# Performance work log

Measured on AMD Instinct MI355X. Metric: run time of the kernel, lower is better.

## Reference

```python
import jax, jax.numpy as jnp
import numpy as np


def _pairwise_dist(x, y):
    # x: [B, N, D], y: [B, M, D] -> [B, N, M] Euclidean distances.
    # Use ||x||^2 + ||y||^2 - 2<x,y> (gram form) to avoid the [B,N,M,D]
    # broadcast intermediate the torch code materializes.
    x2 = jnp.sum(x * x, axis=-1)  # [B, N]
    y2 = jnp.sum(y * y, axis=-1)  # [B, M]
    xy = jnp.einsum('bnd,bmd->bnm', x, y)  # [B, N, M]
    sq = x2[:, :, None] + y2[:, None, :] - 2.0 * xy
    return jnp.sqrt(jnp.maximum(sq, 1e-12))


def setup_inputs() -> dict:
    key = jax.random.key(0)
    k1, k2 = jax.random.split(key)
    B, N, M, D = 8, 4096, 4096, 64
    pred = jax.random.normal(k1, (B, N, D), dtype=jnp.float32)
    label = jax.random.normal(k2, (B, M, D), dtype=jnp.float32)
    return {"pred": pred, "label": label}


def reference(pred, label):
    dis = _pairwise_dist(pred, label)  # [B, N, M]
    dis_xy = jnp.max(jnp.min(dis, axis=2))  # max over all (b, n) of min over m
    dis_yx = jnp.max(jnp.min(dis, axis=1))  # max over all (b, m) of min over n
    return dis_xy + dis_yx
```

## Files before the change

kernel.cpp:

```cpp
#include <hip/hip_runtime.h>
#include <hip/hip_bf16.h>

#define B_ 8
#define N_ 4096
#define M_ 4096
#define D_ 64
#define BNT (B_ * N_)
#define BMT (B_ * M_)
#define TA 128
#define TB 128
#define CHUNK_TILES 8
#define CHUNK_B (TB * CHUNK_TILES)
#define MCHUNK (M_ / CHUNK_B)

typedef short bf16x8 __attribute__((ext_vector_type(8)));
typedef float f32x4 __attribute__((ext_vector_type(4)));

__device__ __forceinline__ unsigned short f2bf(float f) {
  __hip_bfloat16 h = __float2bfloat16(f);
  return *reinterpret_cast<unsigned short*>(&h);
}

__device__ __forceinline__ unsigned fkey(float f) {
  unsigned b = __float_as_uint(f);
  return b ^ ((unsigned)((int)b >> 31) | 0x80000000u);
}
__device__ __forceinline__ float funkey(unsigned k) {
  unsigned b = (k & 0x80000000u) ? (k ^ 0x80000000u) : ~k;
  return __uint_as_float(b);
}

__device__ __forceinline__ bf16x8 cvt8(float4 lo, float4 hi) {
  union { unsigned short u[8]; bf16x8 v; } r;
  r.u[0] = f2bf(lo.x); r.u[1] = f2bf(lo.y); r.u[2] = f2bf(lo.z); r.u[3] = f2bf(lo.w);
  r.u[4] = f2bf(hi.x); r.u[5] = f2bf(hi.y); r.u[6] = f2bf(hi.z); r.u[7] = f2bf(hi.w);
  return r.v;
}

__device__ __forceinline__ void gload_lds16(const void* g, void* l) {
  __builtin_amdgcn_global_load_lds(
      (const __attribute__((address_space(1))) unsigned int*)g,
      (__attribute__((address_space(3))) unsigned int*)l, 16, 0, 0);
}

template <int ROWS, bool BF>
__device__ __forceinline__ void stage_tile(const void* gsrc, unsigned short* lds,
                                           int t, int srcpat) {
  if (BF) {
    constexpr int PER_WAVE = (ROWS * 128 / 1024) / 4;
    const char* gp = (const char*)gsrc;
    int w = t >> 6;
#pragma unroll
    for (int i = 0; i < PER_WAVE; i++) {
      int q = w * PER_WAVE + i;
      gload_lds16(gp + q * 1024 + srcpat, (char*)lds + q * 1024);
    }
  } else {
    const float4* g4 = (const float4*)gsrc;
#pragma unroll
    for (int i = 0; i < ROWS * 16 / 256; i++) {
      int off = i * 256 + t;
      float4 v = g4[off];
      int row = off >> 4;
      int cb = (off & 15) * 8;
      int ba = (row * 128 + cb) ^ ((row & 7) << 4);
      ushort4 p;
      p.x = f2bf(v.x); p.y = f2bf(v.y); p.z = f2bf(v.z); p.w = f2bf(v.w);
      *(ushort4*)((char*)lds + ba) = p;
    }
  }
}

template <bool CONV>
__global__ __launch_bounds__(256) void prep_kernel(
    const float* __restrict__ pred, const float* __restrict__ label,
    unsigned short* __restrict__ predbf, unsigned short* __restrict__ labelbf,
    float* __restrict__ x2, float* __restrict__ y2,
    unsigned* __restrict__ minN, unsigned* __restrict__ minM,
    unsigned* __restrict__ gmax) {
  int t = threadIdx.x;
  int lane = t & 15;
  long row = (long)blockIdx.x * 16 + (t >> 4);
  bool isA = row < BNT;
  const float4* src;
  unsigned short* bdst;
  float* ndst;
  unsigned* mdst;
  if (isA) {
    src = (const float4*)(pred + row * D_);
    bdst = predbf + row * D_;
    ndst = x2 + row;
    mdst = minN + row;
  } else {
    long r2 = row - BNT;
    src = (const float4*)(label + r2 * D_);
    bdst = labelbf + r2 * D_;
    ndst = y2 + r2;
    mdst = minM + r2;
  }
  float4 v = src[lane];
  if (CONV) {
    float s = isA ? -2.f : 1.f;
    ushort4 p;
    p.x = f2bf(s * v.x); p.y = f2bf(s * v.y);
    p.z = f2bf(s * v.z); p.w = f2bf(s * v.w);
    *(ushort4*)(bdst + lane * 4) = p;
  }
  float s = v.x * v.x + v.y * v.y + v.z * v.z + v.w * v.w;
  s += __shfl_xor(s, 1);
  s += __shfl_xor(s, 2);
  s += __shfl_xor(s, 4);
  s += __shfl_xor(s, 8);
  if (lane == 0) {
    *ndst = s;
    *mdst = 0xFFFFFFFFu;
  }
  if (blockIdx.x == 0 && t < 2) gmax[t] = 0u;
}

template <bool BF>
__global__ __launch_bounds__(256) void fused_kernel(
    const void* __restrict__ Asrc, const void* __restrict__ Bsrc,
    const float* __restrict__ x2g, const float* __restrict__ y2g,
    unsigned* __restrict__ minN, unsigned* __restrict__ minM) {
  __shared__ alignas(16) unsigned short Bs[2][TB * 64];
  __shared__ float y2l[CHUNK_B];
  __shared__ float cmSlab[2][CHUNK_B];
  __shared__ float red[2][TA];

  const int t = threadIdx.x;
  const int b = blockIdx.z;
  const int a0 = blockIdx.x * TA;
  const int m0 = blockIdx.y * CHUNK_B;
  const int w = t >> 6, l = t & 63;
  const int g = l >> 4, c = l & 15;
  const int wr = w >> 1, wc = w & 1;
  const int srcpat = (l >> 3) * 128 + (((l & 7) * 16) ^ ((l >> 3) << 4));

  const size_t rowbytes = BF ? 128 : 256;
  const char* Bgl = (const char*)Bsrc + ((size_t)b * M_ + m0) * rowbytes;

  ((float4*)y2l)[t] = ((const float4*)(y2g + (size_t)b * M_ + m0))[t];

  stage_tile<TB, BF>(Bgl, Bs[0], t, srcpat);

  bf16x8 af[2][4];
  if (BF) {
    const unsigned short* Ab =
        (const unsigned short*)Asrc + ((size_t)b * N_ + a0) * D_;
#pragma unroll
    for (int kk = 0; kk < 2; kk++)
#pragma unroll
      for (int mi = 0; mi < 4; mi++)
        af[kk][mi] =
            *(const bf16x8*)(Ab + (size_t)(wr * 64 + mi * 16 + c) * D_ + kk * 32 + g * 8);
  } else {
    const float* Af = (const float*)Asrc + ((size_t)b * N_ + a0) * D_;
#pragma unroll
    for (int kk = 0; kk < 2; kk++)
#pragma unroll
      for (int mi = 0; mi < 4; mi++) {
        const float4* p =
            (const float4*)(Af + (size_t)(wr * 64 + mi * 16 + c) * D_ + kk * 32 + g * 8);
        float4 lo = p[0], hi = p[1];
        lo.x *= -2.f; lo.y *= -2.f; lo.z *= -2.f; lo.w *= -2.f;
        hi.x *= -2.f; hi.y *= -2.f; hi.z *= -2.f; hi.w *= -2.f;
        af[kk][mi] = cvt8(lo, hi);
      }
  }

  float x2v[4][4];
#pragma unroll
  for (int mi = 0; mi < 4; mi++)
#pragma unroll
    for (int e = 0; e < 4; e++)
      x2v[mi][e] = x2g[(size_t)b * N_ + a0 + wr * 64 + mi * 16 + g * 4 + e];

  float rmin[4][4];
#pragma unroll
  for (int mi = 0; mi < 4; mi++)
#pragma unroll
    for (int e = 0; e < 4; e++) rmin[mi][e] = INFINITY;

  __syncthreads();

#pragma unroll
  for (int it = 0; it < CHUNK_TILES; it++) {
    if (it + 1 < CHUNK_TILES)
      stage_tile<TB, BF>(Bgl + (size_t)(it + 1) * TB * rowbytes,
                         Bs[(it + 1) & 1], t, srcpat);
    const char* Bcur = (const char*)Bs[it & 1];

    float nbv[4];
#pragma unroll
    for (int ni = 0; ni < 4; ni++)
      nbv[ni] = y2l[it * TB + wc * 64 + ni * 16 + c];

#pragma unroll
    for (int h = 0; h < 2; h++) {
      bf16x8 b0[2], b1[2];
#pragma unroll
      for (int nj = 0; nj < 2; nj++) {
        int r = wc * 64 + (h * 2 + nj) * 16 + c;
        b0[nj] = *(const bf16x8*)(Bcur + ((r * 128 + g * 16) ^ ((r & 7) << 4)));
        b1[nj] = *(const bf16x8*)(Bcur + ((r * 128 + 64 + g * 16) ^ ((r & 7) << 4)));
      }
      f32x4 acc[4][2];
#pragma unroll
      for (int mi = 0; mi < 4; mi++)
#pragma unroll
        for (int nj = 0; nj < 2; nj++) {
          float nv = nbv[h * 2 + nj];
          acc[mi][nj] = (f32x4){nv, nv, nv, nv};
        }
#pragma unroll
      for (int mi = 0; mi < 4; mi++)
#pragma unroll
        for (int nj = 0; nj < 2; nj++)
          acc[mi][nj] = __builtin_amdgcn_mfma_f32_16x16x32_bf16(
              af[0][mi], b0[nj], acc[mi][nj], 0, 0, 0);
#pragma unroll
      for (int mi = 0; mi < 4; mi++)
#pragma unroll
        for (int nj = 0; nj < 2; nj++)
          acc[mi][nj] = __builtin_amdgcn_mfma_f32_16x16x32_bf16(
              af[1][mi], b1[nj], acc[mi][nj], 0, 0, 0);

#pragma unroll
      for (int nj = 0; nj < 2; nj++) {
        float cm = INFINITY;
#pragma unroll
        for (int mi = 0; mi < 4; mi++)
#pragma unroll
          for (int e = 0; e < 4; e++) {
            float v = acc[mi][nj][e];
            rmin[mi][e] = fminf(rmin[mi][e], v);
            cm = fminf(cm, v + x2v[mi][e]);
          }
        cm = fminf(cm, __shfl_xor(cm, 16));
        cm = fminf(cm, __shfl_xor(cm, 32));
        if (g == 0)
          cmSlab[wr][it * TB + wc * 64 + (h * 2 + nj) * 16 + c] =
              cm - nbv[h * 2 + nj];
      }
    }
    __syncthreads();
  }

#pragma unroll
  for (int mi = 0; mi < 4; mi++)
#pragma unroll
    for (int e = 0; e < 4; e++) {
      float r = rmin[mi][e];
      r = fminf(r, __shfl_xor(r, 1));
      r = fminf(r, __shfl_xor(r, 2));
      r = fminf(r, __shfl_xor(r, 4));
      r = fminf(r, __shfl_xor(r, 8));
      rmin[mi][e] = r;
    }
  if (c == 0) {
#pragma unroll
    for (int mi = 0; mi < 4; mi++)
#pragma unroll
      for (int e = 0; e < 4; e++)
        red[wc][wr * 64 + mi * 16 + g * 4 + e] = rmin[mi][e];
  }
  __syncthreads();
  if (t < TA) {
    float m = fminf(red[0][t], red[1][t]);
    atomicMin(&minN[(size_t)b * N_ + a0 + t], fkey(m));
  }
#pragma unroll
  for (int i = 0; i < CHUNK_B / 256; i++) {
    int r = i * 256 + t;
    float v = fminf(cmSlab[0][r], cmSlab[1][r]);
    atomicMin(&minM[(size_t)b * M_ + m0 + r], fkey(v));
  }
}

__global__ __launch_bounds__(256) void final1_kernel(
    const unsigned* __restrict__ minN, const unsigned* __restrict__ minM,
    const float* __restrict__ x2, const float* __restrict__ y2,
    unsigned* __restrict__ gmax) {
  int dir = blockIdx.x >> 5;
  int blk = blockIdx.x & 31;
  const unsigned* src = dir ? minM : minN;
  const float* nrm = dir ? y2 : x2;
  size_t base = (size_t)blk * 256;
  float mx = -INFINITY;
  {
    int i = threadIdx.x;
    uint4 k = ((const uint4*)src)[base + i];
    float4 nv = ((const float4*)nrm)[base + i];
    mx = fmaxf(mx, nv.x + funkey(k.x));
    mx = fmaxf(mx, nv.y + funkey(k.y));
    mx = fmaxf(mx, nv.z + funkey(k.z));
    mx = fmaxf(mx, nv.w + funkey(k.w));
  }
#pragma unroll
  for (int mask = 1; mask < 64; mask <<= 1) mx = fmaxf(mx, __shfl_xor(mx, mask));
  __shared__ float sm[4];
  if ((threadIdx.x & 63) == 0) sm[threadIdx.x >> 6] = mx;
  __syncthreads();
  if (threadIdx.x == 0) {
    mx = fmaxf(fmaxf(sm[0], sm[1]), fmaxf(sm[2], sm[3]));
    atomicMax(&gmax[dir], fkey(mx));
  }
}

__global__ void final2_kernel(const unsigned* __restrict__ gmax, float* __restrict__ out) {
  if (threadIdx.x == 0)
    out[0] = sqrtf(fmaxf(funkey(gmax[0]), 1e-12f)) +
             sqrtf(fmaxf(funkey(gmax[1]), 1e-12f));
}

extern "C" void kernel_launch(void* const* d_in, const int* in_sizes, int n_in,
                              void* d_out, int out_size, void* d_ws, size_t ws_size,
                              hipStream_t stream) {
  const float* pred = (const float*)d_in[0];
  const float* label = (const float*)d_in[1];
  char* ws = (char*)d_ws;

  const size_t bfBytes = (size_t)BNT * D_ * 2;
  const size_t needFast = 2 * bfBytes + (size_t)(BNT + BMT) * 8 + 64;

  if (ws_size >= needFast) {
    unsigned short* predbf = (unsigned short*)ws;
    unsigned short* labelbf = (unsigned short*)(ws + bfBytes);
    float* x2 = (float*)(ws + 2 * bfBytes);
    float* y2 = x2 + BNT;
    unsigned* minN = (unsigned*)(y2 + BMT);
    unsigned* minM = minN + BNT;
    unsigned* gmax = minM + BMT;

    prep_kernel<true><<<(BNT + BMT) / 16, 256, 0, stream>>>(
        pred, label, predbf, labelbf, x2, y2, minN, minM, gmax);
    fused_kernel<true><<<dim3(N_ / TA, MCHUNK, B_), 256, 0, stream>>>(
        predbf, labelbf, x2, y2, minN, minM);
    final1_kernel<<<64, 256, 0, stream>>>(minN, minM, x2, y2, gmax);
    final2_kernel<<<1, 64, 0, stream>>>(gmax, (float*)d_out);
  } else {
    float* x2 = (float*)ws;
    float* y2 = x2 + BNT;
    unsigned* minN = (unsigned*)(y2 + BMT);
    unsigned* minM = minN + BNT;
    unsigned* gmax = minM + BMT;

    prep_kernel<false><<<(BNT + BMT) / 16, 256, 0, stream>>>(
        pred, label, nullptr, nullptr, x2, y2, minN, minM, gmax);
    fused_kernel<false><<<dim3(N_ / TA, MCHUNK, B_), 256, 0, stream>>>(
        pred, label, x2, y2, minN, minM);
    final1_kernel<<<64, 256, 0, stream>>>(minN, minM, x2, y2, gmax);
    final2_kernel<<<1, 64, 0, stream>>>(gmax, (float*)d_out);
  }
}
```

Before: 69.29 us.

## Remap fused kernel to 512 threads with per-wave column strips over 64-row tile

```diff
diff --git a/kernel.cpp b/kernel.cpp
--- a/kernel.cpp
+++ b/kernel.cpp
@@ -7,8 +7,9 @@
 #define D_ 64
 #define BNT (B_ * N_)
 #define BMT (B_ * M_)
-#define TA 128
+#define TA 64
 #define TB 128
+#define NT 512
 #define CHUNK_TILES 8
 #define CHUNK_B (TB * CHUNK_TILES)
 #define MCHUNK (M_ / CHUNK_B)
@@ -47,7 +48,7 @@
 __device__ __forceinline__ void stage_tile(const void* gsrc, unsigned short* lds,
                                            int t, int srcpat) {
   if (BF) {
-    constexpr int PER_WAVE = (ROWS * 128 / 1024) / 4;
+    constexpr int PER_WAVE = (ROWS * 128 / 1024) / (NT / 64);
     const char* gp = (const char*)gsrc;
     int w = t >> 6;
 #pragma unroll
@@ -58,8 +59,8 @@
   } else {
     const float4* g4 = (const float4*)gsrc;
 #pragma unroll
-    for (int i = 0; i < ROWS * 16 / 256; i++) {
-      int off = i * 256 + t;
+    for (int i = 0; i < ROWS * 16 / NT; i++) {
+      int off = i * NT + t;
       float4 v = g4[off];
       int row = off >> 4;
       int cb = (off & 15) * 8;
@@ -119,14 +120,14 @@
 }
 
 template <bool BF>
-__global__ __launch_bounds__(256) void fused_kernel(
+__global__ __launch_bounds__(NT) void fused_kernel(
     const void* __restrict__ Asrc, const void* __restrict__ Bsrc,
     const float* __restrict__ x2g, const float* __restrict__ y2g,
     unsigned* __restrict__ minN, unsigned* __restrict__ minM) {
   __shared__ alignas(16) unsigned short Bs[2][TB * 64];
   __shared__ float y2l[CHUNK_B];
-  __shared__ float cmSlab[2][CHUNK_B];
-  __shared__ float red[2][TA];
+  __shared__ float cmSlab[CHUNK_B];
+  __shared__ float red[8][TA];
 
   const int t = threadIdx.x;
   const int b = blockIdx.z;
@@ -134,13 +135,12 @@
   const int m0 = blockIdx.y * CHUNK_B;
   const int w = t >> 6, l = t & 63;
   const int g = l >> 4, c = l & 15;
-  const int wr = w >> 1, wc = w & 1;
   const int srcpat = (l >> 3) * 128 + (((l & 7) * 16) ^ ((l >> 3) << 4));
 
   const size_t rowbytes = BF ? 128 : 256;
   const char* Bgl = (const char*)Bsrc + ((size_t)b * M_ + m0) * rowbytes;
 
-  ((float4*)y2l)[t] = ((const float4*)(y2g + (size_t)b * M_ + m0))[t];
+  ((float2*)y2l)[t] = ((const float2*)(y2g + (size_t)b * M_ + m0))[t];
 
   stage_tile<TB, BF>(Bgl, Bs[0], t, srcpat);
 
@@ -153,7 +153,7 @@
 #pragma unroll
       for (int mi = 0; mi < 4; mi++)
         af[kk][mi] =
-            *(const bf16x8*)(Ab + (size_t)(wr * 64 + mi * 16 + c) * D_ + kk * 32 + g * 8);
+            *(const bf16x8*)(Ab + (size_t)(mi * 16 + c) * D_ + kk * 32 + g * 8);
   } else {
     const float* Af = (const float*)Asrc + ((size_t)b * N_ + a0) * D_;
 #pragma unroll
@@ -161,7 +161,7 @@
 #pragma unroll
       for (int mi = 0; mi < 4; mi++) {
         const float4* p =
-            (const float4*)(Af + (size_t)(wr * 64 + mi * 16 + c) * D_ + kk * 32 + g * 8);
+            (const float4*)(Af + (size_t)(mi * 16 + c) * D_ + kk * 32 + g * 8);
         float4 lo = p[0], hi = p[1];
         lo.x *= -2.f; lo.y *= -2.f; lo.z *= -2.f; lo.w *= -2.f;
         hi.x *= -2.f; hi.y *= -2.f; hi.z *= -2.f; hi.w *= -2.f;
@@ -174,7 +174,7 @@
   for (int mi = 0; mi < 4; mi++)
 #pragma unroll
     for (int e = 0; e < 4; e++)
-      x2v[mi][e] = x2g[(size_t)b * N_ + a0 + wr * 64 + mi * 16 + g * 4 + e];
+      x2v[mi][e] = x2g[(size_t)b * N_ + a0 + mi * 16 + g * 4 + e];
 
   float rmin[4][4];
 #pragma unroll
@@ -184,66 +184,44 @@
 
   __syncthreads();
 
-#pragma unroll
   for (int it = 0; it < CHUNK_TILES; it++) {
     if (it + 1 < CHUNK_TILES)
       stage_tile<TB, BF>(Bgl + (size_t)(it + 1) * TB * rowbytes,
                          Bs[(it + 1) & 1], t, srcpat);
-    const char* Bcur = (const char*)Bs[it & 1];
-
-    float nbv[4];
-#pragma unroll
-    for (int ni = 0; ni < 4; ni++)
-      nbv[ni] = y2l[it * TB + wc * 64 + ni * 16 + c];
-
-#pragma unroll
-    for (int h = 0; h < 2; h++) {
-      bf16x8 b0[2], b1[2];
-#pragma unroll
-      for (int nj = 0; nj < 2; nj++) {
-        int r = wc * 64 + (h * 2 + nj) * 16 + c;
-        b0[nj] = *(const bf16x8*)(Bcur + ((r * 128 + g * 16) ^ ((r & 7) << 4)));
-        b1[nj] = *(const bf16x8*)(Bcur + ((r * 128 + 64 + g * 16) ^ ((r & 7) << 4)));
-      }
-      f32x4 acc[4][2];
-#pragma unroll
-      for (int mi = 0; mi < 4; mi++)
-#pragma unroll
-        for (int nj = 0; nj < 2; nj++) {
-          float nv = nbv[h * 2 + nj];
-          acc[mi][nj] = (f32x4){nv, nv, nv, nv};
-        }
-#pragma unroll
-      for (int mi = 0; mi < 4; mi++)
-#pragma unroll
-        for (int nj = 0; nj < 2; nj++)
-          acc[mi][nj] = __builtin_amdgcn_mfma_f32_16x16x32_bf16(
-              af[0][mi], b0[nj], acc[mi][nj], 0, 0, 0);
-#pragma unroll
-      for (int mi = 0; mi < 4; mi++)
-#pragma unroll
-        for (int nj = 0; nj < 2; nj++)
-          acc[mi][nj] = __builtin_amdgcn_mfma_f32_16x16x32_bf16(
-              af[1][mi], b1[nj], acc[mi][nj], 0, 0, 0);
-
-#pragma unroll
-      for (int nj = 0; nj < 2; nj++) {
-        float cm = INFINITY;
-#pragma unroll
-        for (int mi = 0; mi < 4; mi++)
-#pragma unroll
-          for (int e = 0; e < 4; e++) {
-            float v = acc[mi][nj][e];
-            rmin[mi][e] = fminf(rmin[mi][e], v);
-            cm = fminf(cm, v + x2v[mi][e]);
-          }
-        cm = fminf(cm, __shfl_xor(cm, 16));
-        cm = fminf(cm, __shfl_xor(cm, 32));
-        if (g == 0)
-          cmSlab[wr][it * TB + wc * 64 + (h * 2 + nj) * 16 + c] =
-              cm - nbv[h * 2 + nj];
-      }
+    const char* Bcur = (const char*)(&Bs[it & 1][0]);
+
+    const int r = w * 16 + c;
+    const float nv = y2l[it * TB + r];
+    bf16x8 b0 = *(const bf16x8*)(Bcur + ((r * 128 + g * 16) ^ ((r & 7) << 4)));
+    bf16x8 b1 = *(const bf16x8*)(Bcur + ((r * 128 + 64 + g * 16) ^ ((r & 7) << 4)));
+
+    f32x4 acc[4];
+#pragma unroll
+    for (int mi = 0; mi < 4; mi++) acc[mi] = (f32x4){nv, nv, nv, nv};
+#pragma unroll
+    for (int mi = 0; mi < 4; mi++)
+      acc[mi] = __builtin_amdgcn_mfma_f32_16x16x32_bf16(af[0][mi], b0, acc[mi], 0, 0, 0);
+#pragma unroll
+    for (int mi = 0; mi < 4; mi++)
+      acc[mi] = __builtin_amdgcn_mfma_f32_16x16x32_bf16(af[1][mi], b1, acc[mi], 0, 0, 0);
+
+    float cs[4];
+#pragma unroll
+    for (int mi = 0; mi < 4; mi++) {
+      float c0 = acc[mi][0] + x2v[mi][0];
+      float c1 = acc[mi][1] + x2v[mi][1];
+      float c2 = acc[mi][2] + x2v[mi][2];
+      float c3 = acc[mi][3] + x2v[mi][3];
+      cs[mi] = fminf(fminf(c0, c1), fminf(c2, c3));
+#pragma unroll
+      for (int e = 0; e < 4; e++)
+        rmin[mi][e] = fminf(rmin[mi][e], acc[mi][e]);
     }
+    float cm = fminf(fminf(cs[0], cs[1]), fminf(cs[2], cs[3]));
+    cm = fminf(cm, __shfl_xor(cm, 16));
+    cm = fminf(cm, __shfl_xor(cm, 32));
+    if (g == 0) cmSlab[it * TB + r] = cm - nv;
+
     __syncthreads();
   }
 
@@ -263,18 +241,19 @@
     for (int mi = 0; mi < 4; mi++)
 #pragma unroll
       for (int e = 0; e < 4; e++)
-        red[wc][wr * 64 + mi * 16 + g * 4 + e] = rmin[mi][e];
+        red[w][mi * 16 + g * 4 + e] = rmin[mi][e];
   }
   __syncthreads();
   if (t < TA) {
-    float m = fminf(red[0][t], red[1][t]);
+    float m = red[0][t];
+#pragma unroll
+    for (int i = 1; i < 8; i++) m = fminf(m, red[i][t]);
     atomicMin(&minN[(size_t)b * N_ + a0 + t], fkey(m));
   }
 #pragma unroll
-  for (int i = 0; i < CHUNK_B / 256; i++) {
-    int r = i * 256 + t;
-    float v = fminf(cmSlab[0][r], cmSlab[1][r]);
-    atomicMin(&minM[(size_t)b * M_ + m0 + r], fkey(v));
+  for (int i = 0; i < CHUNK_B / NT; i++) {
+    int r = i * NT + t;
+    atomicMin(&minM[(size_t)b * M_ + m0 + r], fkey(cmSlab[r]));
   }
 }
 
@@ -335,7 +314,7 @@
 
     prep_kernel<true><<<(BNT + BMT) / 16, 256, 0, stream>>>(
         pred, label, predbf, labelbf, x2, y2, minN, minM, gmax);
-    fused_kernel<true><<<dim3(N_ / TA, MCHUNK, B_), 256, 0, stream>>>(
+    fused_kernel<true><<<dim3(N_ / TA, MCHUNK, B_), NT, 0, stream>>>(
         predbf, labelbf, x2, y2, minN, minM);
     final1_kernel<<<64, 256, 0, stream>>>(minN, minM, x2, y2, gmax);
     final2_kernel<<<1, 64, 0, stream>>>(gmax, (float*)d_out);
@@ -348,7 +327,7 @@
 
     prep_kernel<false><<<(BNT + BMT) / 16, 256, 0, stream>>>(
         pred, label, nullptr, nullptr, x2, y2, minN, minM, gmax);
-    fused_kernel<false><<<dim3(N_ / TA, MCHUNK, B_), 256, 0, stream>>>(
+    fused_kernel<false><<<dim3(N_ / TA, MCHUNK, B_), NT, 0, stream>>>(
         pred, label, x2, y2, minN, minM);
     final1_kernel<<<64, 256, 0, stream>>>(minN, minM, x2, y2, gmax);
     final2_kernel<<<1, 64, 0, stream>>>(gmax, (float*)d_out);
```

Result: slower. 72.76 us (+5.0%).
